# Performance work log

Hardware: AMD Instinct MI355X
Metric: run time of the kernel (lower is better)

Reference implementation:

```python
import jax, jax.numpy as jnp
import numpy as np

N = 50000      # nodes
E = 800000     # edges (before self-loops)
F_IN = 128     # num_node_features
H = 4          # heads
C = 64         # hidden_channels
G = 64         # graphs in batch
OUT = 5


def setup_inputs():
    key = jax.random.key(0)
    ks = jax.random.split(key, 16)
    s = 0.1
    def rn(k, shape, sc=s):
        return jax.random.normal(k, shape, dtype=jnp.float32) * sc
    return {
        "x": rn(ks[0], (N, F_IN), 1.0),
        "edge_index": jax.random.randint(ks[1], (2, E), 0, N, dtype=jnp.int32),
        "batch": jnp.sort(jax.random.randint(ks[2], (N,), 0, G, dtype=jnp.int32)),
        "W1": rn(ks[3], (F_IN, H * C)), "a1s": rn(ks[4], (H, C)), "a1d": rn(ks[5], (H, C)), "b1": jnp.zeros((H * C,), jnp.float32),
        "g1": jnp.ones((H * C,), jnp.float32), "be1": jnp.zeros((H * C,), jnp.float32),
        "W2": rn(ks[6], (H * C, H * C)), "a2s": rn(ks[7], (H, C)), "a2d": rn(ks[8], (H, C)), "b2": jnp.zeros((H * C,), jnp.float32),
        "g2": jnp.ones((H * C,), jnp.float32), "be2": jnp.zeros((H * C,), jnp.float32),
        "W3": rn(ks[9], (H * C, C)), "a3s": rn(ks[10], (1, C)), "a3d": rn(ks[11], (1, C)), "b3": jnp.zeros((C,), jnp.float32),
        "g3": jnp.ones((C,), jnp.float32), "be3": jnp.zeros((C,), jnp.float32),
        "Wg": rn(ks[12], (C, 128)), "bg": jnp.zeros((128,), jnp.float32),
        "Wg2": rn(ks[13], (128, 64)), "bg2": jnp.zeros((64,), jnp.float32),
        "Wo": rn(ks[14], (64, OUT)), "bo": jnp.zeros((OUT,), jnp.float32),
    }


def _layer_norm(x, g, b, eps=1e-5):
    mu = jnp.mean(x, axis=-1, keepdims=True)
    var = jnp.mean((x - mu) ** 2, axis=-1, keepdims=True)
    return (x - mu) * jax.lax.rsqrt(var + eps) * g + b


def _gat_conv(x, src, dst, W, a_s, a_d, b, heads, c, concat):
    # PyG GATConv (eval mode, dropout inactive): linear -> per-edge scores ->
    # segment softmax over incoming edges of each dst -> scatter-sum aggregation.
    n = x.shape[0]
    h = (x @ W).reshape(n, heads, c)                 # [N,H,C]
    alpha_src = jnp.sum(h * a_s, axis=-1)            # [N,H]
    alpha_dst = jnp.sum(h * a_d, axis=-1)            # [N,H]
    e = jax.nn.leaky_relu(alpha_src[src] + alpha_dst[dst], 0.2)   # [E',H]
    emax = jax.ops.segment_max(e, dst, num_segments=n)            # [N,H]
    ex = jnp.exp(e - emax[dst])
    denom = jax.ops.segment_sum(ex, dst, num_segments=n)
    alpha = ex / denom[dst]                          # softmax per dst (self-loops guarantee denom>0)
    out = jax.ops.segment_sum(alpha[:, :, None] * h[src], dst, num_segments=n)  # [N,H,C]
    out = out.reshape(n, heads * c) if concat else out.mean(axis=1)
    return out + b


def reference(x, edge_index, batch, W1, a1s, a1d, b1, g1, be1, W2, a2s, a2d, b2, g2, be2, W3, a3s, a3d, b3, g3, be3, Wg, bg, Wg2, bg2, Wo, bo):
    n = x.shape[0]
    loop = jnp.arange(n, dtype=edge_index.dtype)
    src = jnp.concatenate([edge_index[0], loop])     # GATConv adds self-loops
    dst = jnp.concatenate([edge_index[1], loop])
    h = _gat_conv(x, src, dst, W1, a1s, a1d, b1, H, C, True)
    h = jax.nn.elu(_layer_norm(h, g1, be1))
    h = _gat_conv(h, src, dst, W2, a2s, a2d, b2, H, C, True)
    h = jax.nn.elu(_layer_norm(h, g2, be2))
    h = _gat_conv(h, src, dst, W3, a3s, a3d, b3, 1, C, False)
    h = jax.nn.elu(_layer_norm(h, g3, be3))
    # global_mean_pool over graph ids
    sums = jax.ops.segment_sum(h, batch, num_segments=G)
    cnt = jax.ops.segment_sum(jnp.ones((n,), h.dtype), batch, num_segments=G)
    gm = sums / jnp.maximum(cnt, 1.0)[:, None]
    z = jax.nn.relu(gm @ Wg + bg)
    z = jax.nn.relu(z @ Wg2 + bg2)
    return z @ Wo + bo
```

## Files before the change

kernel.cpp:

```cpp
#include <hip/hip_runtime.h>
#include <math.h>

typedef _Float16 half2v __attribute__((ext_vector_type(2)));
typedef _Float16 half4v __attribute__((ext_vector_type(4)));
typedef _Float16 half8v __attribute__((ext_vector_type(8)));
typedef float floatx4 __attribute__((ext_vector_type(4)));

static __device__ __forceinline__ half2v pack_rtz(float a, float b) {
  return __builtin_bit_cast(half2v, __builtin_amdgcn_cvt_pkrtz(a, b));
}
static __device__ __forceinline__ float dot2(half2v w, unsigned hi, unsigned lo, unsigned sel, float acc) {
  return __builtin_amdgcn_fdot2(w, __builtin_bit_cast(half2v, __builtin_amdgcn_perm(hi, lo, sel)), acc, false);
}

__global__ __launch_bounds__(256) void prep_kernel(const float* __restrict__ W1,
                                                   const float* __restrict__ W2,
                                                   const float* __restrict__ W3,
                                                   const float* __restrict__ x,
                                                   _Float16* __restrict__ Wt1,
                                                   _Float16* __restrict__ Wt2,
                                                   _Float16* __restrict__ Wt3,
                                                   _Float16* __restrict__ x16, int n8,
                                                   const int* __restrict__ ei, int E, int N,
                                                   int* __restrict__ counts, int ncvt) {
  int b = blockIdx.x;
  int t = threadIdx.x;
  if (b < 256) {
    if (t < 128) Wt1[(size_t)b * 128 + t] = (_Float16)W1[(size_t)t * 256 + b];
  } else if (b < 512) {
    int col = b - 256;
    Wt2[(size_t)col * 256 + t] = (_Float16)W2[(size_t)t * 256 + col];
  } else if (b < 576) {
    int col = b - 512;
    Wt3[(size_t)col * 256 + t] = (_Float16)W3[(size_t)t * 64 + col];
  } else if (b < 576 + ncvt) {
    int i = (b - 576) * 256 + t;
    if (i < n8) {
      float4 a = ((const float4*)x)[2 * i];
      float4 c = ((const float4*)x)[2 * i + 1];
      half8v h = {(_Float16)a.x, (_Float16)a.y, (_Float16)a.z, (_Float16)a.w,
                  (_Float16)c.x, (_Float16)c.y, (_Float16)c.z, (_Float16)c.w};
      ((half8v*)x16)[i] = h;
    }
  } else {
    int e = (b - 576 - ncvt) * 256 + t;
    if (e < E + N) {
      int d = (e < E) ? ei[E + e] : (e - E);
      atomicAdd(&counts[d], 1);
    }
  }
}

__global__ __launch_bounds__(1024) void scan1_kernel(const int* __restrict__ counts,
                                                     int* __restrict__ offsets,
                                                     int* __restrict__ blocksums, int n) {
  __shared__ int wsum[16];
  int tid = threadIdx.x, lane = tid & 63, wid = tid >> 6;
  int i = blockIdx.x * 1024 + tid;
  int v = (i < n) ? counts[i] : 0;
  int x = v;
  #pragma unroll
  for (int off = 1; off < 64; off <<= 1) {
    int t = __shfl_up(x, off);
    if (lane >= off) x += t;
  }
  if (lane == 63) wsum[wid] = x;
  __syncthreads();
  if (wid == 0) {
    int w = (lane < 16) ? wsum[lane] : 0;
    #pragma unroll
    for (int off = 1; off < 16; off <<= 1) {
      int t = __shfl_up(w, off);
      if (lane >= off) w += t;
    }
    if (lane < 16) wsum[lane] = w;
  }
  __syncthreads();
  int wpre = (wid > 0) ? wsum[wid - 1] : 0;
  if (i < n) offsets[i] = wpre + x - v;
  if (tid == 0) blocksums[blockIdx.x] = wsum[15];
}

__global__ __launch_bounds__(1024) void scan2_kernel(int* __restrict__ blocksums,
                                                     int* __restrict__ offsets, int nb, int n) {
  __shared__ int wsum[16];
  int tid = threadIdx.x, lane = tid & 63, wid = tid >> 6;
  int v = (tid < nb) ? blocksums[tid] : 0;
  int x = v;
  #pragma unroll
  for (int off = 1; off < 64; off <<= 1) {
    int t = __shfl_up(x, off);
    if (lane >= off) x += t;
  }
  if (lane == 63) wsum[wid] = x;
  __syncthreads();
  if (wid == 0) {
    int w = (lane < 16) ? wsum[lane] : 0;
    #pragma unroll
    for (int off = 1; off < 16; off <<= 1) {
      int t = __shfl_up(w, off);
      if (lane >= off) w += t;
    }
    if (lane < 16) wsum[lane] = w;
  }
  __syncthreads();
  int wpre = (wid > 0) ? wsum[wid - 1] : 0;
  if (tid < nb) blocksums[tid] = wpre + x - v;
  if (tid == 0) offsets[n] = wsum[15];
}

__global__ void scan3_kernel(int* __restrict__ offsets, int* __restrict__ cursor,
                             const int* __restrict__ blocksums, int n) {
  int i = blockIdx.x * 256 + threadIdx.x;
  if (i < n) {
    int o = offsets[i] + blocksums[i >> 10];
    offsets[i] = o;
    cursor[i] = o;
  }
}

__global__ void scatter_kernel(const int* __restrict__ ei, int E, int N,
                               int* __restrict__ cursor, int* __restrict__ src_csr) {
  int e = blockIdx.x * 256 + threadIdx.x;
  if (e >= E + N) return;
  int s = (e < E) ? ei[e] : (e - E);
  int d = (e < E) ? ei[E + e] : (e - E);
  int pos = atomicAdd(&cursor[d], 1);
  src_csr[pos] = s;
}

template <int NT, int H>
__global__ __launch_bounds__(256) void gemm16_kernel(const _Float16* __restrict__ A,
                                                     const _Float16* __restrict__ Wt,
                                                     const float* __restrict__ als,
                                                     const float* __restrict__ ald,
                                                     _Float16* __restrict__ out16,
                                                     float* __restrict__ asrc,
                                                     float* __restrict__ adst,
                                                     int M, int K) {
  constexpr int Nc = NT * 16;
  constexpr int BM = 128, BK = 32;
  constexpr int CPH = NT / H;
  __shared__ _Float16 As[BM][40];
  __shared__ _Float16 Ws[Nc][40];
  int bm = blockIdx.x * BM;
  int tid = threadIdx.x;
  int w = tid >> 6, l = tid & 63;
  int lr = l & 15, lg = l >> 4;

  floatx4 acc[2][NT];
  #pragma unroll
  for (int nf = 0; nf < 2; ++nf)
    #pragma unroll
    for (int ct = 0; ct < NT; ++ct) acc[nf][ct] = (floatx4){0.f, 0.f, 0.f, 0.f};

  for (int k0 = 0; k0 < K; k0 += BK) {
    #pragma unroll
    for (int i = 0; i < 2; ++i) {
      int idx = tid + i * 256;
      int r = idx >> 2, c8 = idx & 3;
      int gr = bm + r;
      half8v hv = {(_Float16)0, (_Float16)0, (_Float16)0, (_Float16)0,
                   (_Float16)0, (_Float16)0, (_Float16)0, (_Float16)0};
      if (gr < M) hv = *(const half8v*)&A[(size_t)gr * K + k0 + c8 * 8];
      *(half8v*)&As[r][c8 * 8] = hv;
    }
    #pragma unroll
    for (int i = 0; i < NT / 4; ++i) {
      int idx = tid + i * 256;
      int col = idx >> 2, c8 = idx & 3;
      *(half8v*)&Ws[col][c8 * 8] = *(const half8v*)&Wt[(size_t)col * K + k0 + c8 * 8];
    }
    __syncthreads();
    half8v b0 = *(half8v*)&As[w * 32 + lr][lg * 8];
    half8v b1 = *(half8v*)&As[w * 32 + 16 + lr][lg * 8];
    #pragma unroll
    for (int ct = 0; ct < NT; ++ct) {
      half8v a = *(half8v*)&Ws[ct * 16 + lr][lg * 8];
      acc[0][ct] = __builtin_amdgcn_mfma_f32_16x16x32_f16(a, b0, acc[0][ct], 0, 0, 0);
      acc[1][ct] = __builtin_amdgcn_mfma_f32_16x16x32_f16(a, b1, acc[1][ct], 0, 0, 0);
    }
    __syncthreads();
  }
  float4 als4[NT], ald4[NT];
  #pragma unroll
  for (int ct = 0; ct < NT; ++ct) {
    als4[ct] = *(const float4*)&als[ct * 16 + lg * 4];
    ald4[ct] = *(const float4*)&ald[ct * 16 + lg * 4];
  }
  #pragma unroll
  for (int nf = 0; nf < 2; ++nf) {
    int node = bm + w * 32 + nf * 16 + lr;
    float ps[H], pd[H];
    #pragma unroll
    for (int hh = 0; hh < H; ++hh) {
      float s = 0.f, d = 0.f;
      #pragma unroll
      for (int c2 = 0; c2 < CPH; ++c2) {
        int ct = hh * CPH + c2;
        s += acc[nf][ct][0] * als4[ct].x + acc[nf][ct][1] * als4[ct].y +
             acc[nf][ct][2] * als4[ct].z + acc[nf][ct][3] * als4[ct].w;
        d += acc[nf][ct][0] * ald4[ct].x + acc[nf][ct][1] * ald4[ct].y +
             acc[nf][ct][2] * ald4[ct].z + acc[nf][ct][3] * ald4[ct].w;
      }
      ps[hh] = s; pd[hh] = d;
    }
    #pragma unroll
    for (int hh = 0; hh < H; ++hh) {
      ps[hh] += __shfl_xor(ps[hh], 16); ps[hh] += __shfl_xor(ps[hh], 32);
      pd[hh] += __shfl_xor(pd[hh], 16); pd[hh] += __shfl_xor(pd[hh], 32);
    }
    if (node < M) {
      if (lg == 0) {
        #pragma unroll
        for (int hh = 0; hh < H; ++hh) asrc[node * H + hh] = ps[hh];
      } else if (lg == 1) {
        #pragma unroll
        for (int hh = 0; hh < H; ++hh) adst[node * H + hh] = pd[hh];
      }
      #pragma unroll
      for (int ct = 0; ct < NT; ++ct) {
        half4v hv = {(_Float16)acc[nf][ct][0], (_Float16)acc[nf][ct][1],
                     (_Float16)acc[nf][ct][2], (_Float16)acc[nf][ct][3]};
        *(half4v*)&out16[(size_t)node * Nc + ct * 16 + lg * 4] = hv;
      }
    }
  }
}

__global__ __launch_bounds__(128) void agg4_ln_kernel(const _Float16* __restrict__ h16,
                                                      const float* __restrict__ asrc,
                                                      const float* __restrict__ adst,
                                                      const int* __restrict__ offsets,
                                                      const int* __restrict__ src_csr,
                                                      const float* __restrict__ bias,
                                                      const float* __restrict__ g,
                                                      const float* __restrict__ be,
                                                      _Float16* __restrict__ out, int n) {
  int wid = threadIdx.x >> 6, lane = threadIdx.x & 63;
  int node = blockIdx.x * 2 + wid;
  if (node >= n) return;
  int start = offsets[node], end = offsets[node + 1];
  int hl = lane >> 5;
  int l5 = lane & 31;
  int head = l5 >> 3;
  float adh = adst[node * 4 + head];
  const uint4* h4 = (const uint4*)h16;
  const half2v ones = {(_Float16)1.f, (_Float16)1.f};
  float acc[8] = {0.f, 0.f, 0.f, 0.f, 0.f, 0.f, 0.f, 0.f};
  float denom = 0.f;
  int i = start + hl;
  for (; i + 6 < end; i += 8) {
    int s0 = src_csr[i], s1 = src_csr[i + 2], s2 = src_csr[i + 4], s3 = src_csr[i + 6];
    uint4 x0 = h4[(size_t)s0 * 32 + l5];
    uint4 x1 = h4[(size_t)s1 * 32 + l5];
    uint4 x2 = h4[(size_t)s2 * 32 + l5];
    uint4 x3 = h4[(size_t)s3 * 32 + l5];
    float sc0 = asrc[s0 * 4 + head] + adh;
    float sc1 = asrc[s1 * 4 + head] + adh;
    float sc2 = asrc[s2 * 4 + head] + adh;
    float sc3 = asrc[s3 * 4 + head] + adh;
    sc0 = fmaxf(sc0, 0.2f * sc0);
    sc1 = fmaxf(sc1, 0.2f * sc1);
    sc2 = fmaxf(sc2, 0.2f * sc2);
    sc3 = fmaxf(sc3, 0.2f * sc3);
    half2v wa = pack_rtz(__expf(sc0), __expf(sc1));
    half2v wb = pack_rtz(__expf(sc2), __expf(sc3));
    denom = __builtin_amdgcn_fdot2(wa, ones, denom, false);
    denom = __builtin_amdgcn_fdot2(wb, ones, denom, false);
    acc[0] = dot2(wa, x1.x, x0.x, 0x05040100u, acc[0]);
    acc[1] = dot2(wa, x1.x, x0.x, 0x07060302u, acc[1]);
    acc[2] = dot2(wa, x1.y, x0.y, 0x05040100u, acc[2]);
    acc[3] = dot2(wa, x1.y, x0.y, 0x07060302u, acc[3]);
    acc[4] = dot2(wa, x1.z, x0.z, 0x05040100u, acc[4]);
    acc[5] = dot2(wa, x1.z, x0.z, 0x07060302u, acc[5]);
    acc[6] = dot2(wa, x1.w, x0.w, 0x05040100u, acc[6]);
    acc[7] = dot2(wa, x1.w, x0.w, 0x07060302u, acc[7]);
    acc[0] = dot2(wb, x3.x, x2.x, 0x05040100u, acc[0]);
    acc[1] = dot2(wb, x3.x, x2.x, 0x07060302u, acc[1]);
    acc[2] = dot2(wb, x3.y, x2.y, 0x05040100u, acc[2]);
    acc[3] = dot2(wb, x3.y, x2.y, 0x07060302u, acc[3]);
    acc[4] = dot2(wb, x3.z, x2.z, 0x05040100u, acc[4]);
    acc[5] = dot2(wb, x3.z, x2.z, 0x07060302u, acc[5]);
    acc[6] = dot2(wb, x3.w, x2.w, 0x05040100u, acc[6]);
    acc[7] = dot2(wb, x3.w, x2.w, 0x07060302u, acc[7]);
  }
  for (; i + 2 < end; i += 4) {
    int s0 = src_csr[i], s1 = src_csr[i + 2];
    uint4 x0 = h4[(size_t)s0 * 32 + l5];
    uint4 x1 = h4[(size_t)s1 * 32 + l5];
    float sc0 = asrc[s0 * 4 + head] + adh;
    float sc1 = asrc[s1 * 4 + head] + adh;
    sc0 = fmaxf(sc0, 0.2f * sc0);
    sc1 = fmaxf(sc1, 0.2f * sc1);
    half2v wa = pack_rtz(__expf(sc0), __expf(sc1));
    denom = __builtin_amdgcn_fdot2(wa, ones, denom, false);
    acc[0] = dot2(wa, x1.x, x0.x, 0x05040100u, acc[0]);
    acc[1] = dot2(wa, x1.x, x0.x, 0x07060302u, acc[1]);
    acc[2] = dot2(wa, x1.y, x0.y, 0x05040100u, acc[2]);
    acc[3] = dot2(wa, x1.y, x0.y, 0x07060302u, acc[3]);
    acc[4] = dot2(wa, x1.z, x0.z, 0x05040100u, acc[4]);
    acc[5] = dot2(wa, x1.z, x0.z, 0x07060302u, acc[5]);
    acc[6] = dot2(wa, x1.w, x0.w, 0x05040100u, acc[6]);
    acc[7] = dot2(wa, x1.w, x0.w, 0x07060302u, acc[7]);
  }
  if (i < end) {
    int s0 = src_csr[i];
    uint4 x0 = h4[(size_t)s0 * 32 + l5];
    float sc0 = asrc[s0 * 4 + head] + adh;
    sc0 = fmaxf(sc0, 0.2f * sc0);
    half2v wa = pack_rtz(__expf(sc0), 0.f);
    denom = __builtin_amdgcn_fdot2(wa, ones, denom, false);
    acc[0] = dot2(wa, x0.x, x0.x, 0x05040100u, acc[0]);
    acc[1] = dot2(wa, x0.x, x0.x, 0x07060302u, acc[1]);
    acc[2] = dot2(wa, x0.y, x0.y, 0x05040100u, acc[2]);
    acc[3] = dot2(wa, x0.y, x0.y, 0x07060302u, acc[3]);
    acc[4] = dot2(wa, x0.z, x0.z, 0x05040100u, acc[4]);
    acc[5] = dot2(wa, x0.z, x0.z, 0x07060302u, acc[5]);
    acc[6] = dot2(wa, x0.w, x0.w, 0x05040100u, acc[6]);
    acc[7] = dot2(wa, x0.w, x0.w, 0x07060302u, acc[7]);
  }
  #pragma unroll
  for (int j = 0; j < 8; ++j) acc[j] += __shfl_xor(acc[j], 32);
  denom += __shfl_xor(denom, 32);
  float inv = 1.f / denom;
  float o[8];
  float4 b0 = *(const float4*)&bias[l5 * 8];
  float4 b1 = *(const float4*)&bias[l5 * 8 + 4];
  o[0] = acc[0] * inv + b0.x; o[1] = acc[1] * inv + b0.y;
  o[2] = acc[2] * inv + b0.z; o[3] = acc[3] * inv + b0.w;
  o[4] = acc[4] * inv + b1.x; o[5] = acc[5] * inv + b1.y;
  o[6] = acc[6] * inv + b1.z; o[7] = acc[7] * inv + b1.w;
  float s = 0.f;
  #pragma unroll
  for (int j = 0; j < 8; ++j) s += o[j];
  #pragma unroll
  for (int off = 16; off; off >>= 1) s += __shfl_xor(s, off);
  float mu = s * (1.f / 256.f);
  float var = 0.f;
  #pragma unroll
  for (int j = 0; j < 8; ++j) { float d = o[j] - mu; var += d * d; }
  #pragma unroll
  for (int off = 16; off; off >>= 1) var += __shfl_xor(var, off);
  float r = rsqrtf(var * (1.f / 256.f) + 1e-5f);
  float4 g0 = *(const float4*)&g[l5 * 8];
  float4 g1 = *(const float4*)&g[l5 * 8 + 4];
  float4 e0 = *(const float4*)&be[l5 * 8];
  float4 e1 = *(const float4*)&be[l5 * 8 + 4];
  float gg[8] = {g0.x, g0.y, g0.z, g0.w, g1.x, g1.y, g1.z, g1.w};
  float ee[8] = {e0.x, e0.y, e0.z, e0.w, e1.x, e1.y, e1.z, e1.w};
  if (hl == 0) {
    half8v yv;
    #pragma unroll
    for (int j = 0; j < 8; ++j) {
      float t = (o[j] - mu) * r * gg[j] + ee[j];
      t = (t > 0.f) ? t : expm1f(t);
      yv[j] = (_Float16)t;
    }
    *(half8v*)&out[(size_t)node * 256 + l5 * 8] = yv;
  }
}

__global__ __launch_bounds__(128) void agg1_ln_kernel(const _Float16* __restrict__ h16,
                                                      const float* __restrict__ asrc,
                                                      const float* __restrict__ adst,
                                                      const int* __restrict__ offsets,
                                                      const int* __restrict__ src_csr,
                                                      const float* __restrict__ bias,
                                                      const float* __restrict__ g,
                                                      const float* __restrict__ be,
                                                      float* __restrict__ out, int n) {
  int wid = threadIdx.x >> 6, lane = threadIdx.x & 63;
  int node = blockIdx.x * 2 + wid;
  if (node >= n) return;
  int start = offsets[node], end = offsets[node + 1];
  int qi = lane >> 4;
  int ql = lane & 15;
  float adh = adst[node];
  const uint2* h2 = (const uint2*)h16;
  const half2v ones = {(_Float16)1.f, (_Float16)1.f};
  float acc[4] = {0.f, 0.f, 0.f, 0.f};
  float denom = 0.f;
  int i = start + qi;
  for (; i + 12 < end; i += 16) {
    int s0 = src_csr[i], s1 = src_csr[i + 4], s2 = src_csr[i + 8], s3 = src_csr[i + 12];
    uint2 x0 = h2[(size_t)s0 * 16 + ql];
    uint2 x1 = h2[(size_t)s1 * 16 + ql];
    uint2 x2 = h2[(size_t)s2 * 16 + ql];
    uint2 x3 = h2[(size_t)s3 * 16 + ql];
    float sc0 = asrc[s0] + adh;
    float sc1 = asrc[s1] + adh;
    float sc2 = asrc[s2] + adh;
    float sc3 = asrc[s3] + adh;
    sc0 = fmaxf(sc0, 0.2f * sc0);
    sc1 = fmaxf(sc1, 0.2f * sc1);
    sc2 = fmaxf(sc2, 0.2f * sc2);
    sc3 = fmaxf(sc3, 0.2f * sc3);
    half2v wa = pack_rtz(__expf(sc0), __expf(sc1));
    half2v wb = pack_rtz(__expf(sc2), __expf(sc3));
    denom = __builtin_amdgcn_fdot2(wa, ones, denom, false);
    denom = __builtin_amdgcn_fdot2(wb, ones, denom, false);
    acc[0] = dot2(wa, x1.x, x0.x, 0x05040100u, acc[0]);
    acc[1] = dot2(wa, x1.x, x0.x, 0x07060302u, acc[1]);
    acc[2] = dot2(wa, x1.y, x0.y, 0x05040100u, acc[2]);
    acc[3] = dot2(wa, x1.y, x0.y, 0x07060302u, acc[3]);
    acc[0] = dot2(wb, x3.x, x2.x, 0x05040100u, acc[0]);
    acc[1] = dot2(wb, x3.x, x2.x, 0x07060302u, acc[1]);
    acc[2] = dot2(wb, x3.y, x2.y, 0x05040100u, acc[2]);
    acc[3] = dot2(wb, x3.y, x2.y, 0x07060302u, acc[3]);
  }
  for (; i + 4 < end; i += 8) {
    int s0 = src_csr[i], s1 = src_csr[i + 4];
    uint2 x0 = h2[(size_t)s0 * 16 + ql];
    uint2 x1 = h2[(size_t)s1 * 16 + ql];
    float sc0 = asrc[s0] + adh;
    float sc1 = asrc[s1] + adh;
    sc0 = fmaxf(sc0, 0.2f * sc0);
    sc1 = fmaxf(sc1, 0.2f * sc1);
    half2v wa = pack_rtz(__expf(sc0), __expf(sc1));
    denom = __builtin_amdgcn_fdot2(wa, ones, denom, false);
    acc[0] = dot2(wa, x1.x, x0.x, 0x05040100u, acc[0]);
    acc[1] = dot2(wa, x1.x, x0.x, 0x07060302u, acc[1]);
    acc[2] = dot2(wa, x1.y, x0.y, 0x05040100u, acc[2]);
    acc[3] = dot2(wa, x1.y, x0.y, 0x07060302u, acc[3]);
  }
  if (i < end) {
    int s0 = src_csr[i];
    uint2 x0 = h2[(size_t)s0 * 16 + ql];
    float sc0 = asrc[s0] + adh;
    sc0 = fmaxf(sc0, 0.2f * sc0);
    half2v wa = pack_rtz(__expf(sc0), 0.f);
    denom = __builtin_amdgcn_fdot2(wa, ones, denom, false);
    acc[0] = dot2(wa, x0.x, x0.x, 0x05040100u, acc[0]);
    acc[1] = dot2(wa, x0.x, x0.x, 0x07060302u, acc[1]);
    acc[2] = dot2(wa, x0.y, x0.y, 0x05040100u, acc[2]);
    acc[3] = dot2(wa, x0.y, x0.y, 0x07060302u, acc[3]);
  }
  #pragma unroll
  for (int off = 32; off >= 16; off >>= 1) {
    #pragma unroll
    for (int j = 0; j < 4; ++j) acc[j] += __shfl_xor(acc[j], off);
    denom += __shfl_xor(denom, off);
  }
  float inv = 1.f / denom;
  float4 b4 = *(const float4*)&bias[ql * 4];
  float o[4];
  o[0] = acc[0] * inv + b4.x; o[1] = acc[1] * inv + b4.y;
  o[2] = acc[2] * inv + b4.z; o[3] = acc[3] * inv + b4.w;
  float s = o[0] + o[1] + o[2] + o[3];
  #pragma unroll
  for (int off = 8; off; off >>= 1) s += __shfl_xor(s, off);
  float mu = s * (1.f / 64.f);
  float var = 0.f;
  #pragma unroll
  for (int j = 0; j < 4; ++j) { float d = o[j] - mu; var += d * d; }
  #pragma unroll
  for (int off = 8; off; off >>= 1) var += __shfl_xor(var, off);
  float r = rsqrtf(var * (1.f / 64.f) + 1e-5f);
  float4 g4 = *(const float4*)&g[ql * 4];
  float4 e4 = *(const float4*)&be[ql * 4];
  float gg[4] = {g4.x, g4.y, g4.z, g4.w};
  float ee[4] = {e4.x, e4.y, e4.z, e4.w};
  float y[4];
  #pragma unroll
  for (int j = 0; j < 4; ++j) {
    float t = (o[j] - mu) * r * gg[j] + ee[j];
    y[j] = (t > 0.f) ? t : expm1f(t);
  }
  if (qi == 0) {
    *(float4*)&out[(size_t)node * 64 + ql * 4] = make_float4(y[0], y[1], y[2], y[3]);
  }
}

__global__ __launch_bounds__(1024) void graph_head_kernel(const float* __restrict__ h,
                                                          const int* __restrict__ batch, int N,
                                                          const float* __restrict__ Wg,
                                                          const float* __restrict__ bg,
                                                          const float* __restrict__ Wg2,
                                                          const float* __restrict__ bg2,
                                                          const float* __restrict__ Wo,
                                                          const float* __restrict__ bo,
                                                          float* __restrict__ out) {
  __shared__ int bounds[2];
  __shared__ float part[64][16][4];
  __shared__ float gm[64];
  __shared__ float z1[128];
  __shared__ float z2[64];
  int g = blockIdx.x;
  int tid = threadIdx.x;
  if (tid < 2) {
    int target = g + tid;
    int lo = 0, hi = N;
    while (lo < hi) {
      int mid = (lo + hi) >> 1;
      if (batch[mid] < target) lo = mid + 1; else hi = mid;
    }
    bounds[tid] = lo;
  }
  __syncthreads();
  int lo = bounds[0], hi = bounds[1];
  int sub = tid >> 4, cq = tid & 15;
  float4 acc = make_float4(0.f, 0.f, 0.f, 0.f);
  for (int r = lo + sub; r < hi; r += 64) {
    float4 v = *(const float4*)&h[(size_t)r * 64 + cq * 4];
    acc.x += v.x; acc.y += v.y; acc.z += v.z; acc.w += v.w;
  }
  part[sub][cq][0] = acc.x; part[sub][cq][1] = acc.y;
  part[sub][cq][2] = acc.z; part[sub][cq][3] = acc.w;
  __syncthreads();
  #pragma unroll
  for (int st = 32; st >= 1; st >>= 1) {
    if (sub < st) {
      #pragma unroll
      for (int j = 0; j < 4; ++j) part[sub][cq][j] += part[sub + st][cq][j];
    }
    __syncthreads();
  }
  if (tid < 16) {
    float invc = 1.f / fmaxf((float)(hi - lo), 1.f);
    #pragma unroll
    for (int j = 0; j < 4; ++j) gm[tid * 4 + j] = part[0][tid][j] * invc;
  }
  __syncthreads();
  if (tid < 128) {
    float a = bg[tid];
    for (int k = 0; k < 64; ++k) a += gm[k] * Wg[k * 128 + tid];
    z1[tid] = fmaxf(a, 0.f);
  }
  __syncthreads();
  if (tid < 64) {
    float a = bg2[tid];
    for (int k = 0; k < 128; ++k) a += z1[k] * Wg2[k * 64 + tid];
    z2[tid] = fmaxf(a, 0.f);
  }
  __syncthreads();
  if (tid < 5) {
    float a = bo[tid];
    for (int k = 0; k < 64; ++k) a += z2[k] * Wo[k * 5 + tid];
    out[g * 5 + tid] = a;
  }
}

extern "C" void kernel_launch(void* const* d_in, const int* in_sizes, int n_in,
                              void* d_out, int out_size, void* d_ws, size_t ws_size,
                              hipStream_t stream) {
  const float* x   = (const float*)d_in[0];
  const int* ei    = (const int*)d_in[1];
  const int* batch = (const int*)d_in[2];
  const float* W1  = (const float*)d_in[3];
  const float* a1s = (const float*)d_in[4];
  const float* a1d = (const float*)d_in[5];
  const float* b1  = (const float*)d_in[6];
  const float* g1  = (const float*)d_in[7];
  const float* be1 = (const float*)d_in[8];
  const float* W2  = (const float*)d_in[9];
  const float* a2s = (const float*)d_in[10];
  const float* a2d = (const float*)d_in[11];
  const float* b2  = (const float*)d_in[12];
  const float* g2  = (const float*)d_in[13];
  const float* be2 = (const float*)d_in[14];
  const float* W3  = (const float*)d_in[15];
  const float* a3s = (const float*)d_in[16];
  const float* a3d = (const float*)d_in[17];
  const float* b3  = (const float*)d_in[18];
  const float* g3  = (const float*)d_in[19];
  const float* be3 = (const float*)d_in[20];
  const float* Wg  = (const float*)d_in[21];
  const float* bg  = (const float*)d_in[22];
  const float* Wg2 = (const float*)d_in[23];
  const float* bg2 = (const float*)d_in[24];
  const float* Wo  = (const float*)d_in[25];
  const float* bo  = (const float*)d_in[26];

  const int N = in_sizes[2];
  const int E = in_sizes[1] / 2;
  const int ET = E + N;
  const int G = 64;
  const int NB = (N + 1023) / 1024;

  char* ws = (char*)d_ws;
  size_t off = 0;
  auto carve = [&](size_t bytes) {
    void* p = ws + off;
    off = (off + bytes + 255) & ~(size_t)255;
    return p;
  };
  int* counts    = (int*)carve((size_t)N * 4);
  int* offsets   = (int*)carve((size_t)(N + 1) * 4);
  int* cursor    = (int*)carve((size_t)N * 4);
  int* blocksums = (int*)carve((size_t)NB * 4);
  int* src_csr   = (int*)carve((size_t)ET * 4);
  float* asrc    = (float*)carve((size_t)N * 4 * 4);
  float* adst    = (float*)carve((size_t)N * 4 * 4);
  _Float16* x16  = (_Float16*)carve((size_t)N * 128 * 2);
  _Float16* a16  = (_Float16*)carve((size_t)N * 256 * 2);
  _Float16* h16  = (_Float16*)carve((size_t)N * 256 * 2);
  float* buf3    = (float*)carve((size_t)N * 64 * 4);
  _Float16* Wt1  = (_Float16*)carve((size_t)128 * 256 * 2);
  _Float16* Wt2  = (_Float16*)carve((size_t)256 * 256 * 2);
  _Float16* Wt3  = (_Float16*)carve((size_t)256 * 64 * 2);
  (void)ws_size;

  const int egrid = (ET + 255) / 256;
  const int ngrid2 = (N + 1) / 2;
  const int mblocks = (N + 127) / 128;
  const int ncvt = (N * 16 + 255) / 256;

  hipMemsetAsync(counts, 0, (size_t)N * 4, stream);
  prep_kernel<<<576 + ncvt + egrid, 256, 0, stream>>>(W1, W2, W3, x, Wt1, Wt2, Wt3,
                                                      x16, N * 16, ei, E, N, counts, ncvt);

  scan1_kernel<<<NB, 1024, 0, stream>>>(counts, offsets, blocksums, N);
  scan2_kernel<<<1, 1024, 0, stream>>>(blocksums, offsets, NB, N);
  scan3_kernel<<<(N + 255) / 256, 256, 0, stream>>>(offsets, cursor, blocksums, N);
  scatter_kernel<<<egrid, 256, 0, stream>>>(ei, E, N, cursor, src_csr);

  gemm16_kernel<16, 4><<<mblocks, 256, 0, stream>>>(x16, Wt1, a1s, a1d, h16, asrc, adst, N, 128);
  agg4_ln_kernel<<<ngrid2, 128, 0, stream>>>(h16, asrc, adst, offsets, src_csr, b1, g1, be1, a16, N);

  gemm16_kernel<16, 4><<<mblocks, 256, 0, stream>>>(a16, Wt2, a2s, a2d, h16, asrc, adst, N, 256);
  agg4_ln_kernel<<<ngrid2, 128, 0, stream>>>(h16, asrc, adst, offsets, src_csr, b2, g2, be2, a16, N);

  gemm16_kernel<4, 1><<<mblocks, 256, 0, stream>>>(a16, Wt3, a3s, a3d, h16, asrc, adst, N, 256);
  agg1_ln_kernel<<<ngrid2, 128, 0, stream>>>(h16, asrc, adst, offsets, src_csr, b3, g3, be3, buf3, N);

  graph_head_kernel<<<G, 1024, 0, stream>>>(buf3, batch, N, Wg, bg, Wg2, bg2, Wo, bo,
                                            (float*)d_out);
}
```

Before: 353.3 us.

## Fuse CSR construction into a single cooperative kernel with grid syncs

Replaces the memset, the edge-count pass, the three scan kernels and the scatter kernel with one cooperative kernel. It runs 256 blocks and separates the phases with grid.sync(), and the count phase is removed from prep_kernel. The aim is to cut the launch overhead and the inter-kernel gaps of the CSR build. In exchange, each phase runs on a fixed grid of 256x256 threads with grid-stride loops, which lowers parallelism for the atomic passes, adds grid-barrier cost, and no longer overlaps counting with the weight and x conversion.

```diff
diff --git a/kernel.cpp b/kernel.cpp
--- a/kernel.cpp
+++ b/kernel.cpp
@@ -1,5 +1,8 @@
 #include <hip/hip_runtime.h>
+#include <hip/hip_cooperative_groups.h>
 #include <math.h>
+
+namespace cg = cooperative_groups;
 
 typedef _Float16 half2v __attribute__((ext_vector_type(2)));
 typedef _Float16 half4v __attribute__((ext_vector_type(4)));
@@ -20,9 +23,7 @@
                                                    _Float16* __restrict__ Wt1,
                                                    _Float16* __restrict__ Wt2,
                                                    _Float16* __restrict__ Wt3,
-                                                   _Float16* __restrict__ x16, int n8,
-                                                   const int* __restrict__ ei, int E, int N,
-                                                   int* __restrict__ counts, int ncvt) {
+                                                   _Float16* __restrict__ x16, int n8) {
   int b = blockIdx.x;
   int t = threadIdx.x;
   if (b < 256) {
@@ -33,7 +34,7 @@
   } else if (b < 576) {
     int col = b - 512;
     Wt3[(size_t)col * 256 + t] = (_Float16)W3[(size_t)t * 64 + col];
-  } else if (b < 576 + ncvt) {
+  } else {
     int i = (b - 576) * 256 + t;
     if (i < n8) {
       float4 a = ((const float4*)x)[2 * i];
@@ -42,91 +43,83 @@
                   (_Float16)c.x, (_Float16)c.y, (_Float16)c.z, (_Float16)c.w};
       ((half8v*)x16)[i] = h;
     }
-  } else {
-    int e = (b - 576 - ncvt) * 256 + t;
-    if (e < E + N) {
-      int d = (e < E) ? ei[E + e] : (e - E);
-      atomicAdd(&counts[d], 1);
-    }
-  }
-}
-
-__global__ __launch_bounds__(1024) void scan1_kernel(const int* __restrict__ counts,
-                                                     int* __restrict__ offsets,
-                                                     int* __restrict__ blocksums, int n) {
-  __shared__ int wsum[16];
-  int tid = threadIdx.x, lane = tid & 63, wid = tid >> 6;
-  int i = blockIdx.x * 1024 + tid;
-  int v = (i < n) ? counts[i] : 0;
-  int x = v;
-  #pragma unroll
-  for (int off = 1; off < 64; off <<= 1) {
-    int t = __shfl_up(x, off);
-    if (lane >= off) x += t;
-  }
-  if (lane == 63) wsum[wid] = x;
-  __syncthreads();
-  if (wid == 0) {
-    int w = (lane < 16) ? wsum[lane] : 0;
-    #pragma unroll
-    for (int off = 1; off < 16; off <<= 1) {
-      int t = __shfl_up(w, off);
-      if (lane >= off) w += t;
-    }
-    if (lane < 16) wsum[lane] = w;
-  }
-  __syncthreads();
-  int wpre = (wid > 0) ? wsum[wid - 1] : 0;
-  if (i < n) offsets[i] = wpre + x - v;
-  if (tid == 0) blocksums[blockIdx.x] = wsum[15];
-}
-
-__global__ __launch_bounds__(1024) void scan2_kernel(int* __restrict__ blocksums,
-                                                     int* __restrict__ offsets, int nb, int n) {
-  __shared__ int wsum[16];
-  int tid = threadIdx.x, lane = tid & 63, wid = tid >> 6;
-  int v = (tid < nb) ? blocksums[tid] : 0;
-  int x = v;
-  #pragma unroll
-  for (int off = 1; off < 64; off <<= 1) {
-    int t = __shfl_up(x, off);
-    if (lane >= off) x += t;
-  }
-  if (lane == 63) wsum[wid] = x;
-  __syncthreads();
-  if (wid == 0) {
-    int w = (lane < 16) ? wsum[lane] : 0;
-    #pragma unroll
-    for (int off = 1; off < 16; off <<= 1) {
-      int t = __shfl_up(w, off);
-      if (lane >= off) w += t;
-    }
-    if (lane < 16) wsum[lane] = w;
-  }
-  __syncthreads();
-  int wpre = (wid > 0) ? wsum[wid - 1] : 0;
-  if (tid < nb) blocksums[tid] = wpre + x - v;
-  if (tid == 0) offsets[n] = wsum[15];
-}
-
-__global__ void scan3_kernel(int* __restrict__ offsets, int* __restrict__ cursor,
-                             const int* __restrict__ blocksums, int n) {
-  int i = blockIdx.x * 256 + threadIdx.x;
-  if (i < n) {
+  }
+}
+
+__global__ __launch_bounds__(256) void csr_coop_kernel(const int* __restrict__ ei, int E, int N,
+                                                       int* __restrict__ counts,
+                                                       int* __restrict__ offsets,
+                                                       int* __restrict__ cursor,
+                                                       int* __restrict__ blocksums,
+                                                       int* __restrict__ src_csr) {
+  cg::grid_group grid = cg::this_grid();
+  const int tid = threadIdx.x, b = blockIdx.x;
+  const int gt = b * 256 + tid, gs = gridDim.x * 256;
+  const int ET = E + N;
+  for (int i = gt; i < N; i += gs) counts[i] = 0;
+  grid.sync();
+  for (int e = gt; e < ET; e += gs) {
+    int d = (e < E) ? ei[E + e] : (e - E);
+    atomicAdd(&counts[d], 1);
+  }
+  grid.sync();
+  const int NB1 = (N + 1023) >> 10;
+  if (b < NB1) {
+    __shared__ int wsum[4];
+    int base = b << 10;
+    int v[4]; int s = 0;
+    #pragma unroll
+    for (int j = 0; j < 4; ++j) {
+      int i = base + tid * 4 + j;
+      v[j] = (i < N) ? counts[i] : 0;
+      s += v[j];
+    }
+    int lane = tid & 63, wid = tid >> 6;
+    int x = s;
+    #pragma unroll
+    for (int off = 1; off < 64; off <<= 1) {
+      int t2 = __shfl_up(x, off);
+      if (lane >= off) x += t2;
+    }
+    if (lane == 63) wsum[wid] = x;
+    __syncthreads();
+    int wbase = 0;
+    #pragma unroll
+    for (int wdx = 0; wdx < 4; ++wdx) if (wdx < wid) wbase += wsum[wdx];
+    int run = wbase + x - s;
+    #pragma unroll
+    for (int j = 0; j < 4; ++j) {
+      int i = base + tid * 4 + j;
+      if (i < N) offsets[i] = run;
+      run += v[j];
+    }
+    if (tid == 255) blocksums[b] = run;
+  }
+  grid.sync();
+  if (b == 0 && tid < 64) {
+    int v2 = (tid < NB1) ? blocksums[tid] : 0;
+    int x = v2;
+    #pragma unroll
+    for (int off = 1; off < 64; off <<= 1) {
+      int t2 = __shfl_up(x, off);
+      if (tid >= off) x += t2;
+    }
+    if (tid < NB1) blocksums[tid] = x - v2;
+    if (tid == 63) offsets[N] = x;
+  }
+  grid.sync();
+  for (int i = gt; i < N; i += gs) {
     int o = offsets[i] + blocksums[i >> 10];
     offsets[i] = o;
     cursor[i] = o;
   }
-}
-
-__global__ void scatter_kernel(const int* __restrict__ ei, int E, int N,
-                               int* __restrict__ cursor, int* __restrict__ src_csr) {
-  int e = blockIdx.x * 256 + threadIdx.x;
-  if (e >= E + N) return;
-  int s = (e < E) ? ei[e] : (e - E);
-  int d = (e < E) ? ei[E + e] : (e - E);
-  int pos = atomicAdd(&cursor[d], 1);
-  src_csr[pos] = s;
+  grid.sync();
+  for (int e = gt; e < ET; e += gs) {
+    int s2 = (e < E) ? ei[e] : (e - E);
+    int d = (e < E) ? ei[E + e] : (e - E);
+    int pos = atomicAdd(&cursor[d], 1);
+    src_csr[pos] = s2;
+  }
 }
 
 template <int NT, int H>
@@ -572,8 +565,8 @@
   const float* Wo  = (const float*)d_in[25];
   const float* bo  = (const float*)d_in[26];
 
-  const int N = in_sizes[2];
-  const int E = in_sizes[1] / 2;
+  int N = in_sizes[2];
+  int E = in_sizes[1] / 2;
   const int ET = E + N;
   const int G = 64;
   const int NB = (N + 1023) / 1024;
@@ -601,19 +594,17 @@
   _Float16* Wt3  = (_Float16*)carve((size_t)256 * 64 * 2);
   (void)ws_size;
 
-  const int egrid = (ET + 255) / 256;
   const int ngrid2 = (N + 1) / 2;
   const int mblocks = (N + 127) / 128;
   const int ncvt = (N * 16 + 255) / 256;
 
-  hipMemsetAsync(counts, 0, (size_t)N * 4, stream);
-  prep_kernel<<<576 + ncvt + egrid, 256, 0, stream>>>(W1, W2, W3, x, Wt1, Wt2, Wt3,
-                                                      x16, N * 16, ei, E, N, counts, ncvt);
-
-  scan1_kernel<<<NB, 1024, 0, stream>>>(counts, offsets, blocksums, N);
-  scan2_kernel<<<1, 1024, 0, stream>>>(blocksums, offsets, NB, N);
-  scan3_kernel<<<(N + 255) / 256, 256, 0, stream>>>(offsets, cursor, blocksums, N);
-  scatter_kernel<<<egrid, 256, 0, stream>>>(ei, E, N, cursor, src_csr);
+  prep_kernel<<<576 + ncvt, 256, 0, stream>>>(W1, W2, W3, x, Wt1, Wt2, Wt3, x16, N * 16);
+
+  {
+    void* args[] = {(void*)&ei, (void*)&E, (void*)&N, (void*)&counts, (void*)&offsets,
+                    (void*)&cursor, (void*)&blocksums, (void*)&src_csr};
+    hipLaunchCooperativeKernel((void*)csr_coop_kernel, dim3(256), dim3(256), args, 0, stream);
+  }
 
   gemm16_kernel<16, 4><<<mblocks, 256, 0, stream>>>(x16, Wt1, a1s, a1d, h16, asrc, adst, N, 128);
   agg4_ln_kernel<<<ngrid2, 128, 0, stream>>>(h16, asrc, adst, offsets, src_csr, b1, g1, be1, a16, N);
```

Result: slower. 482.1 us (+36.5%).
